# Optimization experiments

Hardware: AMD Instinct MI355X
Metric: run time of the kernel (lower is better)

The kernel has to match this reference:

```python
import jax, jax.numpy as jnp
import numpy as np

B, N, E = 8192, 54, 144
F_NODE, F_EDGE, H, OUT = 18, 5, 48, 80
L = 3  # gnn_layers
LN_EPS = 1e-5


def mish(x):
    return x * jnp.tanh(jax.nn.softplus(x))


def setup_inputs() -> dict:
    key = jax.random.key(0)
    ks = jax.random.split(key, 24)
    s = 0.05
    inp = {
        "node_features": jax.random.normal(ks[0], (B, N, F_NODE), jnp.float32),
        "edge_features": jax.random.normal(ks[1], (B, E, F_EDGE), jnp.float32),
        # input projections
        "w_node": jax.random.normal(ks[2], (F_NODE, H), jnp.float32) * s,
        "b_node": jnp.zeros((H,), jnp.float32),
        "w_edge": jax.random.normal(ks[3], (F_EDGE, H), jnp.float32) * s,
        "b_edge": jnp.zeros((H,), jnp.float32),
        # stacked per-layer params (leading dim = L)
        "msg_w1": jax.random.normal(ks[4], (L, 3 * H, H), jnp.float32) * s,
        "msg_b1": jnp.zeros((L, H), jnp.float32),
        "msg_w2": jax.random.normal(ks[5], (L, H, H), jnp.float32) * s,
        "msg_b2": jnp.zeros((L, H), jnp.float32),
        "upd_w1": jax.random.normal(ks[6], (L, 2 * H, H), jnp.float32) * s,
        "upd_b1": jnp.zeros((L, H), jnp.float32),
        "upd_w2": jax.random.normal(ks[7], (L, H, H), jnp.float32) * s,
        "upd_b2": jnp.zeros((L, H), jnp.float32),
        "ln_g": jnp.ones((L, H), jnp.float32),
        "ln_b": jnp.zeros((L, H), jnp.float32),
        # output projection
        "w_out1": jax.random.normal(ks[8], (2 * H, OUT), jnp.float32) * s,
        "b_out1": jnp.zeros((OUT,), jnp.float32),
        "w_out2": jax.random.normal(ks[9], (OUT, OUT), jnp.float32) * s,
        "b_out2": jnp.zeros((OUT,), jnp.float32),
        "edge_index": jax.random.randint(ks[10], (2, E), 0, N, jnp.int64)
        if jax.config.jax_enable_x64 else jax.random.randint(ks[10], (2, E), 0, N, jnp.int32),
    }
    return inp


def reference(node_features, edge_features, w_node, b_node, w_edge, b_edge,
              msg_w1, msg_b1, msg_w2, msg_b2,
              upd_w1, upd_b1, upd_w2, upd_b2, ln_g, ln_b,
              w_out1, b_out1, w_out2, b_out2, edge_index):
    Bv, Nv, _ = node_features.shape
    Ev = edge_features.shape[1]
    h = mish(node_features @ w_node + b_node)            # [B,N,H]
    e = edge_features @ w_edge + b_edge                  # [B,E,H]
    h_flat = h.reshape(Bv * Nv, H)
    e_flat = e.reshape(Bv * Ev, H)
    offsets = jnp.arange(Bv, dtype=edge_index.dtype) * Nv
    src = (edge_index[0][None, :] + offsets[:, None]).reshape(-1)  # [B*E]
    dst = (edge_index[1][None, :] + offsets[:, None]).reshape(-1)
    for l in range(L):
        m = jnp.concatenate([h_flat[src], h_flat[dst], e_flat], axis=-1)  # [B*E,3H]
        m = mish(m @ msg_w1[l] + msg_b1[l])
        m = mish(m @ msg_w2[l] + msg_b2[l])
        agg = jax.ops.segment_sum(m, dst, num_segments=Bv * Nv)  # scatter-add
        u = jnp.concatenate([h_flat, agg], axis=-1)              # [B*N,2H]
        u = mish(u @ upd_w1[l] + upd_b1[l])
        u = u @ upd_w2[l] + upd_b2[l]
        x = h_flat + u
        mu = jnp.mean(x, axis=-1, keepdims=True)
        var = jnp.mean((x - mu) ** 2, axis=-1, keepdims=True)
        h_flat = (x - mu) * jax.lax.rsqrt(var + LN_EPS) * ln_g[l] + ln_b[l]
    node_emb = h_flat.reshape(Bv, Nv, H)
    mean_pool = node_emb.mean(axis=1)
    max_pool = node_emb.max(axis=1)
    pooled = jnp.concatenate([mean_pool, max_pool], axis=-1)     # [B,2H]
    board_emb = mish(pooled @ w_out1 + b_out1) @ w_out2 + b_out2  # [B,OUT]
    return board_emb, node_emb
```

## Files before the change

kernel.cpp:

```cpp
#include <hip/hip_runtime.h>

#define NGR 8192
#define NN 54
#define NE 144
#define FN 18
#define FE 5
#define HD 48
#define NOUT 80
#define NL 3
#define HS 56
#define MS 72
#define ES 40
#define NFRAG (3 + NL * 33)

typedef short v8s __attribute__((ext_vector_type(8)));
typedef short v4s __attribute__((ext_vector_type(4)));
typedef float v4f __attribute__((ext_vector_type(4)));

#define MFMA(a, bf, c) __builtin_amdgcn_mfma_f32_16x16x32_bf16((a), (bf), (c), 0, 0, 0)

static __device__ __forceinline__ float mish_f(float x) {
  float t = __expf(x);
  float s = 1.0f + t;
  float s2 = s * s;
  float r = (s2 - 1.0f) * __builtin_amdgcn_rcpf(s2 + 1.0f);
  return (x > 20.0f) ? x : x * r;
}
static __device__ __forceinline__ short f2b(float x) {
  union { float f; unsigned u; } v; v.f = x;
  unsigned r = v.u + 0x7FFFu + ((v.u >> 16) & 1u);
  return (short)(r >> 16);
}
static __device__ __forceinline__ float b2f(short s) {
  union { unsigned u; float f; } v; v.u = ((unsigned)(unsigned short)s) << 16;
  return v.f;
}

__global__ void gnn_setup(const float* __restrict__ w_node,
                          const float* __restrict__ w_edge,
                          const float* __restrict__ b_edge,
                          const float* __restrict__ msg_w1,
                          const float* __restrict__ msg_b1,
                          const float* __restrict__ msg_w2,
                          const float* __restrict__ upd_w1,
                          const float* __restrict__ upd_w2,
                          const int* __restrict__ edge_index,
                          int* __restrict__ wsi, float* __restrict__ mb1,
                          short* __restrict__ frags) {
  const int t = threadIdx.x;
  if (blockIdx.x == 0) {
    __shared__ int deg[NN];
    const int* dst = edge_index + NE;
    if (t < NN) {
      int c = 0;
      for (int e = 0; e < NE; ++e) c += (dst[e] == t) ? 1 : 0;
      deg[t] = c;
    }
    __syncthreads();
    if (t == 0) {
      int run = 0;
      for (int n = 0; n < NN; ++n) { wsi[n] = run; run += deg[n]; }
      wsi[NN] = run;
    }
    __syncthreads();
    if (t < NN) {
      int p = wsi[t];
      for (int e = 0; e < NE; ++e)
        if (dst[e] == t) wsi[NN + 1 + (p++)] = e;
    }
    for (int idx = t; idx < NL * HD; idx += 256) {
      int l = idx / HD, c = idx % HD;
      float s = msg_b1[l * HD + c];
      for (int k = 0; k < HD; ++k)
        s += b_edge[k] * msg_w1[(l * 144 + 96 + k) * HD + c];
      mb1[idx] = s;
    }
  }
  for (int eid = blockIdx.x * 256 + t; eid < NFRAG * 512; eid += gridDim.x * 256) {
    int f = eid >> 9, r = eid & 511;
    int lane = r >> 3, j = r & 7;
    int kk = ((lane >> 4) << 3) + j;
    int colq = lane & 15;
    float val = 0.f;
    if (f < 3) {
      int c = f * 16 + colq;
      if (kk < FN) val = w_node[kk * HD + c];
    } else {
      int g = f - 3, l = g / 33, o = g % 33;
      if (o < 9) {
        int ks = o / 3, nt = o % 3, c = nt * 16 + colq, k = ks * 32 + kk;
        val = msg_w1[(l * 144 + k) * HD + c];
      } else if (o < 12) {
        int nt = o - 9, c = nt * 16 + colq;
        if (kk < FE) {
          float s = 0.f;
          for (int k2 = 0; k2 < HD; ++k2)
            s += w_edge[kk * HD + k2] * msg_w1[(l * 144 + 96 + k2) * HD + c];
          val = s;
        }
      } else if (o < 18) {
        int oo = o - 12, ks = oo / 3, nt = oo % 3, c = nt * 16 + colq, k = ks * 32 + kk;
        if (k < HD) val = msg_w2[(l * HD + k) * HD + c];
      } else if (o < 27) {
        int oo = o - 18, ks = oo / 3, nt = oo % 3, c = nt * 16 + colq, k = ks * 32 + kk;
        val = upd_w1[(l * 96 + k) * HD + c];
      } else {
        int oo = o - 27, ks = oo / 3, nt = oo % 3, c = nt * 16 + colq, k = ks * 32 + kk;
        if (k < HD) val = upd_w2[(l * HD + k) * HD + c];
      }
    }
    frags[eid] = f2b(val);
  }
}

__global__ __launch_bounds__(256, 3) void gnn_main(
    const float* __restrict__ nf, const float* __restrict__ efx,
    const float* __restrict__ b_node,
    const float* __restrict__ msg_b2,
    const float* __restrict__ upd_b1, const float* __restrict__ upd_b2,
    const float* __restrict__ ln_g, const float* __restrict__ ln_b,
    const float* __restrict__ w_out1, const float* __restrict__ b_out1,
    const float* __restrict__ w_out2, const float* __restrict__ b_out2,
    const int* __restrict__ edge_index,
    const int* __restrict__ wsi, const float* __restrict__ mb1,
    const short* __restrict__ frags,
    float* __restrict__ out)
{
  __shared__ __align__(16) short h_s[64][HS];
  __shared__ __align__(16) short agg_s[64][HS];
  __shared__ __align__(16) short m_s[NE][MS];
  __shared__ __align__(16) short ef_s[NE][ES];
  __shared__ int src_s[NE], dst_s[NE], off_s[NN + 1], list_s[NE];
  __shared__ float pool_s[2 * HD];
  __shared__ float o1_s[NOUT];

  const int b = blockIdx.x;
  const int t = threadIdx.x;
  const int lane = t & 63;
  const int w = t >> 6;
  const int lx = lane & 15;
  const int lg = (lane >> 4) & 3;
  const int koff = lg << 3;

  if (t < NE) { src_s[t] = edge_index[t] * HS; dst_s[t] = edge_index[NE + t] * HS; }
  if (t < NN + 1) off_s[t] = wsi[t];
  if (t < NE) list_s[t] = wsi[NN + 1 + t];
  for (int idx = t; idx < NE * ES; idx += 256) {
    int r = idx / ES, c = idx % ES;
    ef_s[r][c] = (c < FE) ? f2b(efx[(size_t)b * (NE * FE) + r * FE + c]) : (short)0;
  }
  for (int idx = t; idx < 64 * 32; idx += 256) {
    int r = idx >> 5, c = idx & 31;
    agg_s[r][c] = (r < NN && c < FN) ? f2b(nf[(size_t)b * (NN * FN) + r * FN + c]) : (short)0;
  }
  for (int idx = t; idx < 10 * 16; idx += 256)
    agg_s[54 + (idx >> 4)][32 + (idx & 15)] = 0;
  for (int idx = t; idx < 10 * 48; idx += 256)
    h_s[54 + idx / 48][idx % 48] = 0;
  for (int idx = t; idx < NE * 16; idx += 256)
    m_s[idx >> 4][48 + (idx & 15)] = 0;
  __syncthreads();

  const short* h0 = &h_s[0][0];
  const short* g0 = &agg_s[0][0];
  const short* m0 = &m_s[0][0];

  {
    v8s bw[3];
    #pragma unroll
    for (int nt = 0; nt < 3; ++nt)
      bw[nt] = *(const v8s*)(frags + (size_t)nt * 512 + lane * 8);
    v8s a = *(const v8s*)(g0 + (w * 16 + lx) * HS + koff);
    v4f acc[3];
    #pragma unroll
    for (int nt = 0; nt < 3; ++nt) {
      float bb = b_node[nt * 16 + lx];
      acc[nt] = (v4f){bb, bb, bb, bb};
      acc[nt] = MFMA(a, bw[nt], acc[nt]);
    }
    int orow = w * 16 + lg * 4;
    #pragma unroll
    for (int nt = 0; nt < 3; ++nt)
      #pragma unroll
      for (int r = 0; r < 4; ++r)
        if (orow + r < NN) h_s[orow + r][nt * 16 + lx] = f2b(mish_f(acc[nt][r]));
  }
  __syncthreads();

  for (int l = 0; l < NL; ++l) {
    const short* FB = frags + (size_t)(3 + l * 33) * 512;
    v8s bw1[3][3], bwe[3], bw2[2][3];
    float bm1[3], bm2[3];
    #pragma unroll
    for (int ks = 0; ks < 3; ++ks)
      #pragma unroll
      for (int nt = 0; nt < 3; ++nt)
        bw1[ks][nt] = *(const v8s*)(FB + (size_t)(ks * 3 + nt) * 512 + lane * 8);
    #pragma unroll
    for (int nt = 0; nt < 3; ++nt)
      bwe[nt] = *(const v8s*)(FB + (size_t)(9 + nt) * 512 + lane * 8);
    #pragma unroll
    for (int ks = 0; ks < 2; ++ks)
      #pragma unroll
      for (int nt = 0; nt < 3; ++nt)
        bw2[ks][nt] = *(const v8s*)(FB + (size_t)(12 + ks * 3 + nt) * 512 + lane * 8);
    #pragma unroll
    for (int nt = 0; nt < 3; ++nt) {
      bm1[nt] = mb1[l * HD + nt * 16 + lx];
      bm2[nt] = msg_b2[(size_t)l * HD + nt * 16 + lx];
    }

    for (int mt = w; mt < 9; mt += 4) {
      int e_ = mt * 16 + lx;
      int rs = src_s[e_], rd = dst_s[e_];
      int orow = mt * 16 + lg * 4;
      v4f acc[3];
      v8s ae = *(const v8s*)(&ef_s[0][0] + e_ * ES + koff);
      #pragma unroll
      for (int nt = 0; nt < 3; ++nt) {
        acc[nt] = (v4f){bm1[nt], bm1[nt], bm1[nt], bm1[nt]};
        acc[nt] = MFMA(ae, bwe[nt], acc[nt]);
      }
      #pragma unroll
      for (int ks = 0; ks < 3; ++ks) {
        int kk = ks * 32 + koff;
        const short* ap = (kk < 48) ? (h0 + rs + kk) : (h0 + rd + kk - 48);
        v8s a = *(const v8s*)ap;
        #pragma unroll
        for (int nt = 0; nt < 3; ++nt) acc[nt] = MFMA(a, bw1[ks][nt], acc[nt]);
      }
      #pragma unroll
      for (int nt = 0; nt < 3; ++nt)
        #pragma unroll
        for (int r = 0; r < 4; ++r)
          m_s[orow + r][nt * 16 + lx] = f2b(mish_f(acc[nt][r]));
      const short* mrow = m0 + (mt * 16 + lx) * MS;
      v8s a0 = *(const v8s*)(mrow + koff);
      v8s a1 = *(const v8s*)(mrow + 32 + koff);
      #pragma unroll
      for (int nt = 0; nt < 3; ++nt) {
        acc[nt] = (v4f){bm2[nt], bm2[nt], bm2[nt], bm2[nt]};
        acc[nt] = MFMA(a0, bw2[0][nt], acc[nt]);
        acc[nt] = MFMA(a1, bw2[1][nt], acc[nt]);
      }
      #pragma unroll
      for (int nt = 0; nt < 3; ++nt)
        #pragma unroll
        for (int r = 0; r < 4; ++r)
          m_s[orow + r][nt * 16 + lx] = f2b(mish_f(acc[nt][r]));
    }
    __syncthreads();

    for (int task = t; task < NN * 12; task += 256) {
      int n = task / 12, q = (task % 12) * 4;
      float s0 = 0.f, s1 = 0.f, s2 = 0.f, s3 = 0.f;
      int p1 = off_s[n + 1];
      for (int p = off_s[n]; p < p1; ++p) {
        v4s v = *(const v4s*)(m0 + list_s[p] * MS + q);
        s0 += b2f(v[0]); s1 += b2f(v[1]); s2 += b2f(v[2]); s3 += b2f(v[3]);
      }
      v4s o; o[0] = f2b(s0); o[1] = f2b(s1); o[2] = f2b(s2); o[3] = f2b(s3);
      *(v4s*)(&agg_s[0][0] + n * HS + q) = o;
    }
    __syncthreads();

    {
      v8s u1[3][3], u2[2][3];
      float bu1[3], bu2[3], lg_[3], lb_[3];
      #pragma unroll
      for (int ks = 0; ks < 3; ++ks)
        #pragma unroll
        for (int nt = 0; nt < 3; ++nt)
          u1[ks][nt] = *(const v8s*)(FB + (size_t)(18 + ks * 3 + nt) * 512 + lane * 8);
      #pragma unroll
      for (int ks = 0; ks < 2; ++ks)
        #pragma unroll
        for (int nt = 0; nt < 3; ++nt)
          u2[ks][nt] = *(const v8s*)(FB + (size_t)(27 + ks * 3 + nt) * 512 + lane * 8);
      #pragma unroll
      for (int nt = 0; nt < 3; ++nt) {
        bu1[nt] = upd_b1[(size_t)l * HD + nt * 16 + lx];
        bu2[nt] = upd_b2[(size_t)l * HD + nt * 16 + lx];
        lg_[nt] = ln_g[(size_t)l * HD + nt * 16 + lx];
        lb_[nt] = ln_b[(size_t)l * HD + nt * 16 + lx];
      }
      const int nrow = w * 16 + lx;
      const int orow = w * 16 + lg * 4;
      v4f acc[3];
      #pragma unroll
      for (int nt = 0; nt < 3; ++nt) acc[nt] = (v4f){bu1[nt], bu1[nt], bu1[nt], bu1[nt]};
      #pragma unroll
      for (int ks = 0; ks < 3; ++ks) {
        int kk = ks * 32 + koff;
        const short* ap = (kk < 48) ? (h0 + nrow * HS + kk) : (g0 + nrow * HS + kk - 48);
        v8s a = *(const v8s*)ap;
        #pragma unroll
        for (int nt = 0; nt < 3; ++nt) acc[nt] = MFMA(a, u1[ks][nt], acc[nt]);
      }
      #pragma unroll
      for (int nt = 0; nt < 3; ++nt)
        #pragma unroll
        for (int r = 0; r < 4; ++r)
          m_s[orow + r][nt * 16 + lx] = f2b(mish_f(acc[nt][r]));
      const short* mrow = m0 + nrow * MS;
      v8s a0 = *(const v8s*)(mrow + koff);
      v8s a1 = *(const v8s*)(mrow + 32 + koff);
      #pragma unroll
      for (int nt = 0; nt < 3; ++nt) {
        acc[nt] = (v4f){bu2[nt], bu2[nt], bu2[nt], bu2[nt]};
        acc[nt] = MFMA(a0, u2[0][nt], acc[nt]);
        acc[nt] = MFMA(a1, u2[1][nt], acc[nt]);
      }
      float x[3][4], s[4], q[4];
      #pragma unroll
      for (int r = 0; r < 4; ++r) {
        #pragma unroll
        for (int nt = 0; nt < 3; ++nt)
          x[nt][r] = acc[nt][r] + b2f(h_s[orow + r][nt * 16 + lx]);
        s[r] = x[0][r] + x[1][r] + x[2][r];
        q[r] = x[0][r] * x[0][r] + x[1][r] * x[1][r] + x[2][r] * x[2][r];
      }
      #pragma unroll
      for (int mask = 1; mask <= 8; mask <<= 1)
        #pragma unroll
        for (int r = 0; r < 4; ++r) {
          s[r] += __shfl_xor(s[r], mask);
          q[r] += __shfl_xor(q[r], mask);
        }
      float* onode = out + (size_t)NGR * NOUT + (size_t)b * (NN * HD);
      #pragma unroll
      for (int r = 0; r < 4; ++r) {
        float mu = s[r] * (1.0f / HD);
        float vr = q[r] * (1.0f / HD) - mu * mu;
        float rsg = rsqrtf(vr + 1e-5f);
        int row = orow + r;
        #pragma unroll
        for (int nt = 0; nt < 3; ++nt) {
          float y = (x[nt][r] - mu) * rsg * lg_[nt] + lb_[nt];
          if (row < NN) {
            h_s[row][nt * 16 + lx] = f2b(y);
            if (l == NL - 1) onode[row * HD + nt * 16 + lx] = y;
          }
        }
      }
    }
    __syncthreads();
  }

  if (t < HD) {
    float sm = 0.f, mx = -3.0e38f;
    for (int n = 0; n < NN; ++n) { float v = b2f(h_s[n][t]); sm += v; mx = fmaxf(mx, v); }
    pool_s[t] = sm * (1.0f / NN);
    pool_s[HD + t] = mx;
  }
  __syncthreads();

  if (t < NOUT) {
    float a = b_out1[t];
    #pragma unroll 8
    for (int k = 0; k < 2 * HD; ++k) a += pool_s[k] * w_out1[k * NOUT + t];
    o1_s[t] = mish_f(a);
  }
  __syncthreads();
  if (t < NOUT) {
    float a = b_out2[t];
    #pragma unroll 8
    for (int k = 0; k < NOUT; ++k) a += o1_s[k] * w_out2[k * NOUT + t];
    out[(size_t)b * NOUT + t] = a;
  }
}

extern "C" void kernel_launch(void* const* d_in, const int* in_sizes, int n_in,
                              void* d_out, int out_size, void* d_ws, size_t ws_size,
                              hipStream_t stream) {
  const float* nf     = (const float*)d_in[0];
  const float* ef     = (const float*)d_in[1];
  const float* w_node = (const float*)d_in[2];
  const float* b_node = (const float*)d_in[3];
  const float* w_edge = (const float*)d_in[4];
  const float* b_edge = (const float*)d_in[5];
  const float* msg_w1 = (const float*)d_in[6];
  const float* msg_b1 = (const float*)d_in[7];
  const float* msg_w2 = (const float*)d_in[8];
  const float* msg_b2 = (const float*)d_in[9];
  const float* upd_w1 = (const float*)d_in[10];
  const float* upd_b1 = (const float*)d_in[11];
  const float* upd_w2 = (const float*)d_in[12];
  const float* upd_b2 = (const float*)d_in[13];
  const float* ln_g   = (const float*)d_in[14];
  const float* ln_b   = (const float*)d_in[15];
  const float* w_out1 = (const float*)d_in[16];
  const float* b_out1 = (const float*)d_in[17];
  const float* w_out2 = (const float*)d_in[18];
  const float* b_out2 = (const float*)d_in[19];
  const int* edge_index = (const int*)d_in[20];

  int*   wsi   = (int*)d_ws;
  float* mb1   = (float*)d_ws + 256;
  short* frags = (short*)((char*)d_ws + 2048);

  gnn_setup<<<32, 256, 0, stream>>>(w_node, w_edge, b_edge, msg_w1, msg_b1,
                                    msg_w2, upd_w1, upd_w2, edge_index,
                                    wsi, mb1, frags);
  gnn_main<<<NGR, 256, 0, stream>>>(nf, ef, b_node, msg_b2, upd_b1, upd_b2,
                                    ln_g, ln_b, w_out1, b_out1, w_out2, b_out2,
                                    edge_index, wsi, mb1, frags, (float*)d_out);
}
```

Before: 483.1 us.

## Replace CSR scatter-add with MFMA one-hot aggregation and shrink LDS footprint

Replaces the CSR-based segment-sum over edges with a matrix multiply of the transposed messages against a one-hot destination matrix built in registers, run on MFMA. Message outputs are written transposed so they can serve as MFMA A operands, and the edge features are loaded straight into registers instead of staged in LDS. LDS arrays shrink and occupancy is raised to 4 blocks per SM. Weight fragments are reloaded from global or L2 at each use rather than held in registers, trading extra load traffic for lower register pressure.

New measurement: 483.5 us. About the same (+0.1%).

```diff
diff --git a/kernel.cpp b/kernel.cpp
--- a/kernel.cpp
+++ b/kernel.cpp
@@ -10,14 +10,13 @@
 #define NL 3
 #define HS 56
 #define MS 72
-#define ES 40
-#define NFRAG (3 + NL * 33)
+#define TS 152
+#define NFRAG 102
 
 typedef short v8s __attribute__((ext_vector_type(8)));
-typedef short v4s __attribute__((ext_vector_type(4)));
 typedef float v4f __attribute__((ext_vector_type(4)));
 
-#define MFMA(a, bf, c) __builtin_amdgcn_mfma_f32_16x16x32_bf16((a), (bf), (c), 0, 0, 0)
+#define MFMA(a, b, c) __builtin_amdgcn_mfma_f32_16x16x32_bf16((a), (b), (c), 0, 0, 0)
 
 static __device__ __forceinline__ float mish_f(float x) {
   float t = __expf(x);
@@ -34,6 +33,9 @@
 static __device__ __forceinline__ float b2f(short s) {
   union { unsigned u; float f; } v; v.u = ((unsigned)(unsigned short)s) << 16;
   return v.f;
+}
+static __device__ __forceinline__ unsigned pk2(float a, float b) {
+  return (unsigned)(unsigned short)f2b(a) | ((unsigned)(unsigned short)f2b(b) << 16);
 }
 
 __global__ void gnn_setup(const float* __restrict__ w_node,
@@ -44,30 +46,9 @@
                           const float* __restrict__ msg_w2,
                           const float* __restrict__ upd_w1,
                           const float* __restrict__ upd_w2,
-                          const int* __restrict__ edge_index,
-                          int* __restrict__ wsi, float* __restrict__ mb1,
-                          short* __restrict__ frags) {
+                          float* __restrict__ mb1, short* __restrict__ frags) {
   const int t = threadIdx.x;
   if (blockIdx.x == 0) {
-    __shared__ int deg[NN];
-    const int* dst = edge_index + NE;
-    if (t < NN) {
-      int c = 0;
-      for (int e = 0; e < NE; ++e) c += (dst[e] == t) ? 1 : 0;
-      deg[t] = c;
-    }
-    __syncthreads();
-    if (t == 0) {
-      int run = 0;
-      for (int n = 0; n < NN; ++n) { wsi[n] = run; run += deg[n]; }
-      wsi[NN] = run;
-    }
-    __syncthreads();
-    if (t < NN) {
-      int p = wsi[t];
-      for (int e = 0; e < NE; ++e)
-        if (dst[e] == t) wsi[NN + 1 + (p++)] = e;
-    }
     for (int idx = t; idx < NL * HD; idx += 256) {
       int l = idx / HD, c = idx % HD;
       float s = msg_b1[l * HD + c];
@@ -88,10 +69,10 @@
     } else {
       int g = f - 3, l = g / 33, o = g % 33;
       if (o < 9) {
-        int ks = o / 3, nt = o % 3, c = nt * 16 + colq, k = ks * 32 + kk;
+        int ks = o / 3, ct = o % 3, c = ct * 16 + colq, k = ks * 32 + kk;
         val = msg_w1[(l * 144 + k) * HD + c];
       } else if (o < 12) {
-        int nt = o - 9, c = nt * 16 + colq;
+        int ct = o - 9, c = ct * 16 + colq;
         if (kk < FE) {
           float s = 0.f;
           for (int k2 = 0; k2 < HD; ++k2)
@@ -99,13 +80,13 @@
           val = s;
         }
       } else if (o < 18) {
-        int oo = o - 12, ks = oo / 3, nt = oo % 3, c = nt * 16 + colq, k = ks * 32 + kk;
+        int oo = o - 12, ks = oo / 3, ct = oo % 3, c = ct * 16 + colq, k = ks * 32 + kk;
         if (k < HD) val = msg_w2[(l * HD + k) * HD + c];
       } else if (o < 27) {
-        int oo = o - 18, ks = oo / 3, nt = oo % 3, c = nt * 16 + colq, k = ks * 32 + kk;
+        int oo = o - 18, ks = oo / 3, ct = oo % 3, c = ct * 16 + colq, k = ks * 32 + kk;
         val = upd_w1[(l * 96 + k) * HD + c];
       } else {
-        int oo = o - 27, ks = oo / 3, nt = oo % 3, c = nt * 16 + colq, k = ks * 32 + kk;
+        int oo = o - 27, ks = oo / 3, ct = oo % 3, c = ct * 16 + colq, k = ks * 32 + kk;
         if (k < HD) val = upd_w2[(l * HD + k) * HD + c];
       }
     }
@@ -113,7 +94,7 @@
   }
 }
 
-__global__ __launch_bounds__(256, 3) void gnn_main(
+__global__ __launch_bounds__(256, 4) void gnn_main(
     const float* __restrict__ nf, const float* __restrict__ efx,
     const float* __restrict__ b_node,
     const float* __restrict__ msg_b2,
@@ -122,203 +103,195 @@
     const float* __restrict__ w_out1, const float* __restrict__ b_out1,
     const float* __restrict__ w_out2, const float* __restrict__ b_out2,
     const int* __restrict__ edge_index,
-    const int* __restrict__ wsi, const float* __restrict__ mb1,
-    const short* __restrict__ frags,
+    const float* __restrict__ mb1, const short* __restrict__ frags,
     float* __restrict__ out)
 {
-  __shared__ __align__(16) short h_s[64][HS];
-  __shared__ __align__(16) short agg_s[64][HS];
-  __shared__ __align__(16) short m_s[NE][MS];
-  __shared__ __align__(16) short ef_s[NE][ES];
-  __shared__ int src_s[NE], dst_s[NE], off_s[NN + 1], list_s[NE];
-  __shared__ float pool_s[2 * HD];
-  __shared__ float o1_s[NOUT];
+  __shared__ __align__(16) short h_s[NN][HS];
+  __shared__ __align__(16) short agg_s[NN][HS];
+  __shared__ __align__(16) short m_s[80][MS];
+  __shared__ __align__(16) short m_t[48 * TS + 8];
+  __shared__ int dst_s[NE];
+  __shared__ float psum[96], pmax[96], pooled[96], o1[NOUT];
 
   const int b = blockIdx.x;
   const int t = threadIdx.x;
   const int lane = t & 63;
   const int w = t >> 6;
   const int lx = lane & 15;
-  const int lg = (lane >> 4) & 3;
+  const int lg = lane >> 4;
   const int koff = lg << 3;
-
-  if (t < NE) { src_s[t] = edge_index[t] * HS; dst_s[t] = edge_index[NE + t] * HS; }
-  if (t < NN + 1) off_s[t] = wsi[t];
-  if (t < NE) list_s[t] = wsi[NN + 1 + t];
-  for (int idx = t; idx < NE * ES; idx += 256) {
-    int r = idx / ES, c = idx % ES;
-    ef_s[r][c] = (c < FE) ? f2b(efx[(size_t)b * (NE * FE) + r * FE + c]) : (short)0;
-  }
+  const int lg4 = lg << 2;
+
+#define LD8(f) (*(const v8s*)(frags + ((size_t)(f) << 9) + (lane << 3)))
+
+  if (t < NE) dst_s[t] = edge_index[NE + t];
   for (int idx = t; idx < 64 * 32; idx += 256) {
     int r = idx >> 5, c = idx & 31;
-    agg_s[r][c] = (r < NN && c < FN) ? f2b(nf[(size_t)b * (NN * FN) + r * FN + c]) : (short)0;
-  }
-  for (int idx = t; idx < 10 * 16; idx += 256)
-    agg_s[54 + (idx >> 4)][32 + (idx & 15)] = 0;
-  for (int idx = t; idx < 10 * 48; idx += 256)
-    h_s[54 + idx / 48][idx % 48] = 0;
-  for (int idx = t; idx < NE * 16; idx += 256)
+    m_s[r][c] = (r < NN && c < FN) ? f2b(nf[(size_t)b * (NN * FN) + r * FN + c]) : (short)0;
+  }
+  for (int idx = t; idx < 80 * 16; idx += 256)
     m_s[idx >> 4][48 + (idx & 15)] = 0;
+  for (int idx = t; idx < 48 * 8; idx += 256)
+    m_t[(idx >> 3) * TS + 144 + (idx & 7)] = 0;
+  if (t < 8) m_t[48 * TS + t] = 0;
+
+  const int mt0 = w, mt2 = 5 + w;
+  int rs0 = edge_index[mt0 * 16 + lx] * HS, rd0 = edge_index[NE + mt0 * 16 + lx] * HS;
+  int rs1 = 0, rd1 = 0;
+  if (w == 0) { rs1 = edge_index[64 + lx] * HS; rd1 = edge_index[NE + 64 + lx] * HS; }
+  int rs2 = edge_index[mt2 * 16 + lx] * HS, rd2 = edge_index[NE + mt2 * 16 + lx] * HS;
+
+  auto ldef = [&](int mt) -> v8s {
+    v8s r = {0, 0, 0, 0, 0, 0, 0, 0};
+    if (lg == 0) {
+      const float* ep = efx + (size_t)b * (NE * FE) + (mt * 16 + lx) * FE;
+      r[0] = f2b(ep[0]); r[1] = f2b(ep[1]); r[2] = f2b(ep[2]);
+      r[3] = f2b(ep[3]); r[4] = f2b(ep[4]);
+    }
+    return r;
+  };
+  v8s aef0 = ldef(mt0);
+  v8s aef1 = (w == 0) ? ldef(4) : (v8s){0,0,0,0,0,0,0,0};
+  v8s aef2 = ldef(mt2);
+
   __syncthreads();
 
   const short* h0 = &h_s[0][0];
   const short* g0 = &agg_s[0][0];
-  const short* m0 = &m_s[0][0];
 
   {
-    v8s bw[3];
-    #pragma unroll
-    for (int nt = 0; nt < 3; ++nt)
-      bw[nt] = *(const v8s*)(frags + (size_t)nt * 512 + lane * 8);
-    v8s a = *(const v8s*)(g0 + (w * 16 + lx) * HS + koff);
-    v4f acc[3];
+    v8s a = *(const v8s*)(&m_s[w * 16 + lx][koff]);
+    const int orow = w * 16 + lg4;
     #pragma unroll
     for (int nt = 0; nt < 3; ++nt) {
       float bb = b_node[nt * 16 + lx];
-      acc[nt] = (v4f){bb, bb, bb, bb};
-      acc[nt] = MFMA(a, bw[nt], acc[nt]);
-    }
-    int orow = w * 16 + lg * 4;
-    #pragma unroll
-    for (int nt = 0; nt < 3; ++nt)
+      v4f c = {bb, bb, bb, bb};
+      c = MFMA(a, LD8(nt), c);
       #pragma unroll
       for (int r = 0; r < 4; ++r)
-        if (orow + r < NN) h_s[orow + r][nt * 16 + lx] = f2b(mish_f(acc[nt][r]));
+        if (orow + r < NN) h_s[orow + r][nt * 16 + lx] = f2b(mish_f(c[r]));
+    }
   }
   __syncthreads();
 
   for (int l = 0; l < NL; ++l) {
-    const short* FB = frags + (size_t)(3 + l * 33) * 512;
-    v8s bw1[3][3], bwe[3], bw2[2][3];
+    const int FB = 3 + l * 33;
     float bm1[3], bm2[3];
-    #pragma unroll
-    for (int ks = 0; ks < 3; ++ks)
-      #pragma unroll
-      for (int nt = 0; nt < 3; ++nt)
-        bw1[ks][nt] = *(const v8s*)(FB + (size_t)(ks * 3 + nt) * 512 + lane * 8);
-    #pragma unroll
-    for (int nt = 0; nt < 3; ++nt)
-      bwe[nt] = *(const v8s*)(FB + (size_t)(9 + nt) * 512 + lane * 8);
-    #pragma unroll
-    for (int ks = 0; ks < 2; ++ks)
-      #pragma unroll
-      for (int nt = 0; nt < 3; ++nt)
-        bw2[ks][nt] = *(const v8s*)(FB + (size_t)(12 + ks * 3 + nt) * 512 + lane * 8);
     #pragma unroll
     for (int nt = 0; nt < 3; ++nt) {
       bm1[nt] = mb1[l * HD + nt * 16 + lx];
       bm2[nt] = msg_b2[(size_t)l * HD + nt * 16 + lx];
     }
 
-    for (int mt = w; mt < 9; mt += 4) {
-      int e_ = mt * 16 + lx;
-      int rs = src_s[e_], rd = dst_s[e_];
-      int orow = mt * 16 + lg * 4;
-      v4f acc[3];
-      v8s ae = *(const v8s*)(&ef_s[0][0] + e_ * ES + koff);
-      #pragma unroll
-      for (int nt = 0; nt < 3; ++nt) {
-        acc[nt] = (v4f){bm1[nt], bm1[nt], bm1[nt], bm1[nt]};
-        acc[nt] = MFMA(ae, bwe[nt], acc[nt]);
-      }
+    auto do_msg = [&](int mt, int slot, v8s aef, int rs, int rd) {
+      v4f c0 = {bm1[0], bm1[0], bm1[0], bm1[0]};
+      v4f c1 = {bm1[1], bm1[1], bm1[1], bm1[1]};
+      v4f c2 = {bm1[2], bm1[2], bm1[2], bm1[2]};
+      c0 = MFMA(aef, LD8(FB + 9),  c0);
+      c1 = MFMA(aef, LD8(FB + 10), c1);
+      c2 = MFMA(aef, LD8(FB + 11), c2);
       #pragma unroll
       for (int ks = 0; ks < 3; ++ks) {
         int kk = ks * 32 + koff;
-        const short* ap = (kk < 48) ? (h0 + rs + kk) : (h0 + rd + kk - 48);
-        v8s a = *(const v8s*)ap;
-        #pragma unroll
-        for (int nt = 0; nt < 3; ++nt) acc[nt] = MFMA(a, bw1[ks][nt], acc[nt]);
-      }
-      #pragma unroll
-      for (int nt = 0; nt < 3; ++nt)
-        #pragma unroll
-        for (int r = 0; r < 4; ++r)
-          m_s[orow + r][nt * 16 + lx] = f2b(mish_f(acc[nt][r]));
-      const short* mrow = m0 + (mt * 16 + lx) * MS;
-      v8s a0 = *(const v8s*)(mrow + koff);
-      v8s a1 = *(const v8s*)(mrow + 32 + koff);
+        const short* p = (kk < HD) ? (h0 + rs + kk) : (h0 + rd + (kk - HD));
+        v8s a = *(const v8s*)p;
+        c0 = MFMA(a, LD8(FB + ks * 3 + 0), c0);
+        c1 = MFMA(a, LD8(FB + ks * 3 + 1), c1);
+        c2 = MFMA(a, LD8(FB + ks * 3 + 2), c2);
+      }
+      const int orow = slot + lg4;
+      #pragma unroll
+      for (int r = 0; r < 4; ++r) {
+        m_s[orow + r][lx]      = f2b(mish_f(c0[r]));
+        m_s[orow + r][16 + lx] = f2b(mish_f(c1[r]));
+        m_s[orow + r][32 + lx] = f2b(mish_f(c2[r]));
+      }
+      v8s a0 = *(const v8s*)(&m_s[slot + lx][koff]);
+      v8s a1 = *(const v8s*)(&m_s[slot + lx][32 + koff]);
       #pragma unroll
       for (int nt = 0; nt < 3; ++nt) {
-        acc[nt] = (v4f){bm2[nt], bm2[nt], bm2[nt], bm2[nt]};
-        acc[nt] = MFMA(a0, bw2[0][nt], acc[nt]);
-        acc[nt] = MFMA(a1, bw2[1][nt], acc[nt]);
-      }
-      #pragma unroll
-      for (int nt = 0; nt < 3; ++nt)
-        #pragma unroll
-        for (int r = 0; r < 4; ++r)
-          m_s[orow + r][nt * 16 + lx] = f2b(mish_f(acc[nt][r]));
-    }
+        v4f c = {bm2[nt], bm2[nt], bm2[nt], bm2[nt]};
+        c = MFMA(a0, LD8(FB + 12 + nt), c);
+        c = MFMA(a1, LD8(FB + 15 + nt), c);
+        uint2 u;
+        u.x = pk2(mish_f(c[0]), mish_f(c[1]));
+        u.y = pk2(mish_f(c[2]), mish_f(c[3]));
+        *(uint2*)(&m_t[(nt * 16 + lx) * TS + mt * 16 + lg4]) = u;
+      }
+    };
+    do_msg(mt0, w * 16, aef0, rs0, rd0);
+    if (w == 0) do_msg(4, 64, aef1, rs1, rd1);
+    do_msg(mt2, w * 16, aef2, rs2, rd2);
     __syncthreads();
 
-    for (int task = t; task < NN * 12; task += 256) {
-      int n = task / 12, q = (task % 12) * 4;
-      float s0 = 0.f, s1 = 0.f, s2 = 0.f, s3 = 0.f;
-      int p1 = off_s[n + 1];
-      for (int p = off_s[n]; p < p1; ++p) {
-        v4s v = *(const v4s*)(m0 + list_s[p] * MS + q);
-        s0 += b2f(v[0]); s1 += b2f(v[1]); s2 += b2f(v[2]); s3 += b2f(v[3]);
-      }
-      v4s o; o[0] = f2b(s0); o[1] = f2b(s1); o[2] = f2b(s2); o[3] = f2b(s3);
-      *(v4s*)(&agg_s[0][0] + n * HS + q) = o;
-    }
-    __syncthreads();
-
+    const int node = w * 16 + lx;
     {
-      v8s u1[3][3], u2[2][3];
-      float bu1[3], bu2[3], lg_[3], lb_[3];
-      #pragma unroll
-      for (int ks = 0; ks < 3; ++ks)
-        #pragma unroll
-        for (int nt = 0; nt < 3; ++nt)
-          u1[ks][nt] = *(const v8s*)(FB + (size_t)(18 + ks * 3 + nt) * 512 + lane * 8);
-      #pragma unroll
-      for (int ks = 0; ks < 2; ++ks)
-        #pragma unroll
-        for (int nt = 0; nt < 3; ++nt)
-          u2[ks][nt] = *(const v8s*)(FB + (size_t)(27 + ks * 3 + nt) * 512 + lane * 8);
-      #pragma unroll
-      for (int nt = 0; nt < 3; ++nt) {
-        bu1[nt] = upd_b1[(size_t)l * HD + nt * 16 + lx];
-        bu2[nt] = upd_b2[(size_t)l * HD + nt * 16 + lx];
-        lg_[nt] = ln_g[(size_t)l * HD + nt * 16 + lx];
-        lb_[nt] = ln_b[(size_t)l * HD + nt * 16 + lx];
-      }
-      const int nrow = w * 16 + lx;
-      const int orow = w * 16 + lg * 4;
-      v4f acc[3];
-      #pragma unroll
-      for (int nt = 0; nt < 3; ++nt) acc[nt] = (v4f){bu1[nt], bu1[nt], bu1[nt], bu1[nt]};
+      v8s sfr[5];
+      #pragma unroll
+      for (int kt = 0; kt < 5; ++kt) {
+        v8s sv = {0, 0, 0, 0, 0, 0, 0, 0};
+        #pragma unroll
+        for (int j = 0; j < 8; ++j) {
+          int e = kt * 32 + koff + j;
+          if (e < NE && dst_s[e] == node) sv[j] = (short)0x3F80;
+        }
+        sfr[kt] = sv;
+      }
+      #pragma unroll
+      for (int ct = 0; ct < 3; ++ct) {
+        v4f c = {0.f, 0.f, 0.f, 0.f};
+        #pragma unroll
+        for (int kt = 0; kt < 5; ++kt) {
+          v8s a = *(const v8s*)(&m_t[(ct * 16 + lx) * TS + kt * 32 + koff]);
+          c = MFMA(a, sfr[kt], c);
+        }
+        if (node < NN) {
+          uint2 u; u.x = pk2(c[0], c[1]); u.y = pk2(c[2], c[3]);
+          *(uint2*)(&agg_s[node][ct * 16 + lg4]) = u;
+        }
+      }
+    }
+    {
+      const int nrd = (node < NN) ? node : 0;
+      v4f c0 = {upd_b1[l*HD + lx],      upd_b1[l*HD + lx],      upd_b1[l*HD + lx],      upd_b1[l*HD + lx]};
+      v4f c1 = {upd_b1[l*HD + 16 + lx], upd_b1[l*HD + 16 + lx], upd_b1[l*HD + 16 + lx], upd_b1[l*HD + 16 + lx]};
+      v4f c2 = {upd_b1[l*HD + 32 + lx], upd_b1[l*HD + 32 + lx], upd_b1[l*HD + 32 + lx], upd_b1[l*HD + 32 + lx]};
       #pragma unroll
       for (int ks = 0; ks < 3; ++ks) {
         int kk = ks * 32 + koff;
-        const short* ap = (kk < 48) ? (h0 + nrow * HS + kk) : (g0 + nrow * HS + kk - 48);
-        v8s a = *(const v8s*)ap;
-        #pragma unroll
-        for (int nt = 0; nt < 3; ++nt) acc[nt] = MFMA(a, u1[ks][nt], acc[nt]);
-      }
-      #pragma unroll
-      for (int nt = 0; nt < 3; ++nt)
-        #pragma unroll
-        for (int r = 0; r < 4; ++r)
-          m_s[orow + r][nt * 16 + lx] = f2b(mish_f(acc[nt][r]));
-      const short* mrow = m0 + nrow * MS;
-      v8s a0 = *(const v8s*)(mrow + koff);
-      v8s a1 = *(const v8s*)(mrow + 32 + koff);
+        const short* p = (kk < HD) ? (h0 + nrd * HS + kk) : (g0 + nrd * HS + (kk - HD));
+        v8s a = *(const v8s*)p;
+        c0 = MFMA(a, LD8(FB + 18 + ks * 3 + 0), c0);
+        c1 = MFMA(a, LD8(FB + 18 + ks * 3 + 1), c1);
+        c2 = MFMA(a, LD8(FB + 18 + ks * 3 + 2), c2);
+      }
+      const int orow = w * 16 + lg4;
+      #pragma unroll
+      for (int r = 0; r < 4; ++r) {
+        m_s[orow + r][lx]      = f2b(mish_f(c0[r]));
+        m_s[orow + r][16 + lx] = f2b(mish_f(c1[r]));
+        m_s[orow + r][32 + lx] = f2b(mish_f(c2[r]));
+      }
+      v8s a0 = *(const v8s*)(&m_s[node][koff]);
+      v8s a1 = *(const v8s*)(&m_s[node][32 + koff]);
+      v4f cc[3];
       #pragma unroll
       for (int nt = 0; nt < 3; ++nt) {
-        acc[nt] = (v4f){bu2[nt], bu2[nt], bu2[nt], bu2[nt]};
-        acc[nt] = MFMA(a0, u2[0][nt], acc[nt]);
-        acc[nt] = MFMA(a1, u2[1][nt], acc[nt]);
+        float bb = upd_b2[(size_t)l * HD + nt * 16 + lx];
+        v4f c = {bb, bb, bb, bb};
+        c = MFMA(a0, LD8(FB + 27 + nt), c);
+        c = MFMA(a1, LD8(FB + 30 + nt), c);
+        cc[nt] = c;
       }
       float x[3][4], s[4], q[4];
       #pragma unroll
       for (int r = 0; r < 4; ++r) {
+        int rr = (orow + r < NN) ? (orow + r) : 0;
         #pragma unroll
         for (int nt = 0; nt < 3; ++nt)
-          x[nt][r] = acc[nt][r] + b2f(h_s[orow + r][nt * 16 + lx]);
+          x[nt][r] = cc[nt][r] + b2f(h_s[rr][nt * 16 + lx]);
         s[r] = x[0][r] + x[1][r] + x[2][r];
-        q[r] = x[0][r] * x[0][r] + x[1][r] * x[1][r] + x[2][r] * x[2][r];
+        q[r] = fmaf(x[0][r], x[0][r], fmaf(x[1][r], x[1][r], x[2][r] * x[2][r]));
       }
       #pragma unroll
       for (int mask = 1; mask <= 8; mask <<= 1)
@@ -330,13 +303,13 @@
       float* onode = out + (size_t)NGR * NOUT + (size_t)b * (NN * HD);
       #pragma unroll
       for (int r = 0; r < 4; ++r) {
-        float mu = s[r] * (1.0f / HD);
-        float vr = q[r] * (1.0f / HD) - mu * mu;
-        float rsg = rsqrtf(vr + 1e-5f);
+        float mu = s[r] * (1.f / HD);
+        float var = q[r] * (1.f / HD) - mu * mu;
+        float rsg = rsqrtf(var + 1e-5f);
         int row = orow + r;
         #pragma unroll
         for (int nt = 0; nt < 3; ++nt) {
-          float y = (x[nt][r] - mu) * rsg * lg_[nt] + lb_[nt];
+          float y = (x[nt][r] - mu) * rsg * ln_g[l * HD + nt * 16 + lx] + ln_b[l * HD + nt * 16 + lx];
           if (row < NN) {
             h_s[row][nt * 16 + lx] = f2b(y);
             if (l == NL - 1) onode[row * HD + nt * 16 + lx] = y;
@@ -347,25 +320,35 @@
     __syncthreads();
   }
 
+  if (t < 96) {
+    int half = t >= HD;
+    int ch = t - half * HD;
+    float smv = 0.f, mx = -3.0e38f;
+    int n0 = half * 27;
+    for (int n = n0; n < n0 + 27; ++n) {
+      float v = b2f(h_s[n][ch]);
+      smv += v; mx = fmaxf(mx, v);
+    }
+    psum[t] = smv; pmax[t] = mx;
+  }
+  __syncthreads();
   if (t < HD) {
-    float sm = 0.f, mx = -3.0e38f;
-    for (int n = 0; n < NN; ++n) { float v = b2f(h_s[n][t]); sm += v; mx = fmaxf(mx, v); }
-    pool_s[t] = sm * (1.0f / NN);
-    pool_s[HD + t] = mx;
+    pooled[t] = (psum[t] + psum[HD + t]) * (1.f / NN);
+    pooled[HD + t] = fmaxf(pmax[t], pmax[HD + t]);
   }
   __syncthreads();
 
   if (t < NOUT) {
     float a = b_out1[t];
     #pragma unroll 8
-    for (int k = 0; k < 2 * HD; ++k) a += pool_s[k] * w_out1[k * NOUT + t];
-    o1_s[t] = mish_f(a);
+    for (int k = 0; k < 2 * HD; ++k) a = fmaf(pooled[k], w_out1[k * NOUT + t], a);
+    o1[t] = mish_f(a);
   }
   __syncthreads();
   if (t < NOUT) {
     float a = b_out2[t];
     #pragma unroll 8
-    for (int k = 0; k < NOUT; ++k) a += o1_s[k] * w_out2[k * NOUT + t];
+    for (int k = 0; k < NOUT; ++k) a = fmaf(o1[k], w_out2[k * NOUT + t], a);
     out[(size_t)b * NOUT + t] = a;
   }
 }
@@ -395,14 +378,12 @@
   const float* b_out2 = (const float*)d_in[19];
   const int* edge_index = (const int*)d_in[20];
 
-  int*   wsi   = (int*)d_ws;
-  float* mb1   = (float*)d_ws + 256;
-  short* frags = (short*)((char*)d_ws + 2048);
+  float* mb1   = (float*)d_ws;
+  short* frags = (short*)((char*)d_ws + 1024);
 
   gnn_setup<<<32, 256, 0, stream>>>(w_node, w_edge, b_edge, msg_w1, msg_b1,
-                                    msg_w2, upd_w1, upd_w2, edge_index,
-                                    wsi, mb1, frags);
+                                    msg_w2, upd_w1, upd_w2, mb1, frags);
   gnn_main<<<NGR, 256, 0, stream>>>(nf, ef, b_node, msg_b2, upd_b1, upd_b2,
                                     ln_g, ln_b, w_out1, b_out1, w_out2, b_out2,
-                                    edge_index, wsi, mb1, frags, (float*)d_out);
-}
+                                    edge_index, mb1, frags, (float*)d_out);
+}
```
